# Kernel optimization log

Measured on AMD Instinct MI355X. Metric: run time of the kernel, lower is better.

Reference implementation:

```python
import jax, jax.numpy as jnp
import numpy as np

MUL = 32          # multiplicity of 0e and 1o in edge_messages_irreps
E = 40000         # number of edges
NODE_DIM = 128    # 128x0e node feats
EDGE_DIM = 32     # 32x0e edge feats
WEIGHT_NUMEL = 5 * MUL * MUL  # 5 uvu instructions, (u,v)=(32,32) weights each

# Levi-Civita tensor = sqrt(6) * wigner_3j(1,1,1) in the e3nn real basis
_eps = np.zeros((3, 3, 3), np.float32)
for a, b, c in [(0, 1, 2), (1, 2, 0), (2, 0, 1)]:
    _eps[a, b, c] = 1.0
    _eps[a, c, b] = -1.0
EPS = jnp.asarray(_eps)


def setup_inputs() -> dict:
    key = jax.random.key(0)
    ks = jax.random.split(key, 13)
    return {
        "edge_feats": jax.random.normal(ks[0], (E, EDGE_DIM), jnp.float32),
        "edge_messages1": jax.random.normal(ks[1], (E, 4 * MUL), jnp.float32),
        "edge_messages2": jax.random.normal(ks[2], (E, 4 * MUL), jnp.float32),
        "node_feats_sender": jax.random.normal(ks[3], (E, NODE_DIM), jnp.float32),
        "node_feats_receiver": jax.random.normal(ks[4], (E, NODE_DIM), jnp.float32),
        "W_nodes": jax.random.normal(ks[5], (NODE_DIM, EDGE_DIM), jnp.float32),
        "W_mlp1": jax.random.normal(ks[6], (3 * EDGE_DIM, 128), jnp.float32),
        "W_mlp2": jax.random.normal(ks[7], (128, 128), jnp.float32),
        "W_mlp3": jax.random.normal(ks[8], (128, WEIGHT_NUMEL), jnp.float32),
        "W_out_0e": jax.random.normal(ks[9], (2 * MUL, MUL), jnp.float32),
        "W_out_1o": jax.random.normal(ks[10], (2 * MUL, MUL), jnp.float32),
        "W_out_1e": jax.random.normal(ks[11], (MUL, MUL), jnp.float32),
        "edge_index": jax.random.randint(ks[12], (2, E), 0, 10000, jnp.int64 if jax.config.jax_enable_x64 else jnp.int32),
    }


def reference(edge_feats, edge_messages1, edge_messages2, node_feats_sender,
              node_feats_receiver, W_nodes, W_mlp1, W_mlp2, W_mlp3,
              W_out_0e, W_out_1o, W_out_1e, edge_index):
    # nodes_linear: o3.Linear on pure scalars == dense matmul with 1/sqrt(fan_in)
    s_send = (node_feats_sender @ W_nodes) * (1.0 / np.sqrt(NODE_DIM))
    s_recv = (node_feats_receiver @ W_nodes) * (1.0 / np.sqrt(NODE_DIM))
    scal = jnp.concatenate([s_send, s_recv, edge_feats], axis=1)  # [E, 96]

    # FullyConnectedNet [96,128,128,weight_numel] with SiLU, e3nn fan-in scaling
    h = jax.nn.silu((scal @ W_mlp1) * (1.0 / np.sqrt(3 * EDGE_DIM)))
    h = jax.nn.silu((h @ W_mlp2) * (1.0 / np.sqrt(128)))
    w = (h @ W_mlp3) * (1.0 / np.sqrt(128))          # [E, 5120] per-edge TP weights
    w = w.reshape(-1, 5, MUL, MUL)                    # 5 uvu instructions

    # split messages into 32x0e scalars and 32x1o vectors
    x1_0 = edge_messages1[:, :MUL]
    x1_1 = edge_messages1[:, MUL:].reshape(-1, MUL, 3)
    x2_0 = edge_messages2[:, :MUL]
    x2_1 = edge_messages2[:, MUL:].reshape(-1, MUL, 3)

    # per-edge-weighted uvu tensor product; alpha = sqrt(ir_out.dim / fan) with
    # CG constants (1, d/sqrt(3), eps/sqrt(6)) folded in
    c1 = jnp.einsum('euv,eu,ev->eu', w[:, 0], x1_0, x2_0) * (1.0 / np.sqrt(MUL))          # 0e
    c2 = jnp.einsum('euv,eu,evj->euj', w[:, 1], x1_0, x2_1) * (1.0 / np.sqrt(MUL))        # 1o
    c3 = jnp.einsum('euv,eui,ev->eui', w[:, 2], x1_1, x2_0) * (1.0 / np.sqrt(MUL))        # 1o
    c4 = jnp.einsum('euv,eui,evi->eu', w[:, 3], x1_1, x2_1) * (1.0 / np.sqrt(3 * MUL))    # 0e
    c5 = jnp.einsum('euv,eui,evj,ijk->euk', w[:, 4], x1_1, x2_1, EPS) * (1.0 / np.sqrt(2 * MUL))  # 1e

    # output_linear: o3.Linear over irreps_mid -> 32x0e + 32x1o + 32x1e
    mid_0e = jnp.concatenate([c1, c4], axis=1)        # [E, 64]
    mid_1o = jnp.concatenate([c2, c3], axis=1)        # [E, 64, 3]
    out_0e = (mid_0e @ W_out_0e) * (1.0 / np.sqrt(2 * MUL))                      # [E, 32]
    out_1o = jnp.einsum('euj,uw->ewj', mid_1o, W_out_1o) * (1.0 / np.sqrt(2 * MUL))
    out_1e = jnp.einsum('euk,uw->ewk', c5, W_out_1e) * (1.0 / np.sqrt(MUL))

    n = out_0e.shape[0]
    return jnp.concatenate(
        [out_0e, out_1o.reshape(n, 3 * MUL), out_1e.reshape(n, 3 * MUL)], axis=1)  # [E, 224]
```

## Files before the change

### kernel.cpp

```cpp
#include <hip/hip_runtime.h>
#include <hip/hip_bf16.h>
#include <math.h>

typedef __attribute__((ext_vector_type(8)))  short bf16x8;
typedef __attribute__((ext_vector_type(4)))  float f32x4;
typedef __attribute__((ext_vector_type(16))) float f32x16;

#define S128 0.08838834764831845f
#define S96  0.10206207261596575f
#define S32  0.17677669529663687f
#define S64  0.125f
#define NE   40000

__device__ __forceinline__ float silu_f(float x){ return x / (1.0f + expf(-x)); }
__device__ __forceinline__ ushort f2b(float x){
    __hip_bfloat16 b = __float2bfloat16(x); return *(ushort*)&b;
}
__device__ __forceinline__ float b2f(ushort u){
    return __uint_as_float(((uint)u) << 16);
}
__device__ __forceinline__ float blo(uint d){ return __uint_as_float(d << 16); }
__device__ __forceinline__ float bhi(uint d){ return __uint_as_float(d & 0xffff0000u); }
__device__ __forceinline__ uint packbf(float a, float b){
    return (uint)f2b(a) | ((uint)f2b(b) << 16);
}

__global__ __launch_bounds__(256)
void prep_weights(const float* __restrict__ Wn, const float* __restrict__ W1,
                  const float* __restrict__ W2, ushort* __restrict__ WnT,
                  ushort* __restrict__ W1T, ushort* __restrict__ W2T) {
    int idx = blockIdx.x * 256 + threadIdx.x;
    if (idx < 4096) {
        int n = idx >> 7, k = idx & 127;
        WnT[n * 128 + k] = f2b(Wn[k * 32 + n]);
    } else if (idx < 16384) {
        int t = idx - 4096; int n = t / 96, k = t - n * 96;
        W1T[n * 96 + k] = f2b(W1[k * 128 + n]);
    } else {
        int t = idx - 16384; int n = t >> 7, k = t & 127;
        W2T[n * 128 + k] = f2b(W2[k * 128 + n]);
    }
}

__global__ __launch_bounds__(256)
void w3_fragpack(const float* __restrict__ W3, ushort* __restrict__ w3A) {
    const int pu = blockIdx.x;
    const int t  = threadIdx.x;
    #pragma unroll
    for (int s = 0; s < 2; ++s) {
        int slot = s * 256 + t;
        int ks = slot >> 6, l = slot & 63;
        int m = pu * 32 + (l & 31);
        int kbase = ks * 16 + (l >> 5) * 8;
        bf16x8 v;
        #pragma unroll
        for (int i = 0; i < 8; ++i)
            v[i] = (short)f2b(W3[(size_t)(kbase + i) * 5120 + m]);
        *(bf16x8*)&w3A[((size_t)(pu * 8 + ks) * 64 + l) * 8] = v;
    }
}

__global__ __launch_bounds__(512, 6)
void mega2(const float* __restrict__ ef,  const float* __restrict__ em2,
           const float* __restrict__ nfs, const float* __restrict__ nfr,
           const ushort* __restrict__ WnT, const ushort* __restrict__ W1T,
           const ushort* __restrict__ W2T, const ushort* __restrict__ w3A,
           ushort* __restrict__ dt)
{
    __shared__ __align__(16) ushort scratch[15360];
    __shared__ __align__(16) ushort hbuf[64 * 128];

    const int tid  = threadIdx.x;
    const int lane = tid & 63, wv = tid >> 6;
    const int l15  = lane & 15, lg = lane >> 4;
    const int e0   = blockIdx.x * 64;

    ushort* scal = scratch;
    ushort* h1b  = scratch + 6656;
    uint*   xp2  = (uint*)scratch;

    #pragma unroll
    for (int q = 0; q < 4; ++q) {
        int idx = q * 512 + tid;
        int e = idx >> 5, j = idx & 31;
        scal[e * 104 + 64 + j] = f2b(ef[(size_t)(e0 + e) * 32 + j]);
    }

    {
        const int h = wv >> 2, eb = (wv & 3) * 16;
        const float* src = h ? nfr : nfs;
        const size_t erow = (size_t)(e0 + eb + l15) * 128;
        f32x4 acc1[2] = {{0,0,0,0},{0,0,0,0}};
        #pragma unroll
        for (int ks = 0; ks < 4; ++ks) {
            float4 va = *(const float4*)(src + erow + ks * 32 + lg * 8);
            float4 vb = *(const float4*)(src + erow + ks * 32 + lg * 8 + 4);
            bf16x8 a;
            a[0]=(short)f2b(va.x); a[1]=(short)f2b(va.y);
            a[2]=(short)f2b(va.z); a[3]=(short)f2b(va.w);
            a[4]=(short)f2b(vb.x); a[5]=(short)f2b(vb.y);
            a[6]=(short)f2b(vb.z); a[7]=(short)f2b(vb.w);
            #pragma unroll
            for (int nf = 0; nf < 2; ++nf) {
                bf16x8 b = *(const bf16x8*)(WnT + (nf * 16 + l15) * 128 + ks * 32 + lg * 8);
                acc1[nf] = __builtin_amdgcn_mfma_f32_16x16x32_bf16(a, b, acc1[nf], 0, 0, 0);
            }
        }
        #pragma unroll
        for (int nf = 0; nf < 2; ++nf)
            #pragma unroll
            for (int r = 0; r < 4; ++r)
                scal[(eb + lg * 4 + r) * 104 + h * 32 + nf * 16 + l15] =
                    f2b(acc1[nf][r] * S128);
    }
    __syncthreads();

    {
        const int et = wv & 3, nh = wv >> 2;
        f32x4 acc2[4] = {{0,0,0,0},{0,0,0,0},{0,0,0,0},{0,0,0,0}};
        #pragma unroll
        for (int ks = 0; ks < 3; ++ks) {
            bf16x8 a = *(const bf16x8*)&scal[(et * 16 + l15) * 104 + ks * 32 + lg * 8];
            #pragma unroll
            for (int nf = 0; nf < 4; ++nf) {
                int gn = nh * 4 + nf;
                bf16x8 b = *(const bf16x8*)(W1T + (gn * 16 + l15) * 96 + ks * 32 + lg * 8);
                acc2[nf] = __builtin_amdgcn_mfma_f32_16x16x32_bf16(a, b, acc2[nf], 0, 0, 0);
            }
        }
        #pragma unroll
        for (int nf = 0; nf < 4; ++nf)
            #pragma unroll
            for (int r = 0; r < 4; ++r)
                h1b[(et * 16 + lg * 4 + r) * 136 + (nh * 4 + nf) * 16 + l15] =
                    f2b(silu_f(acc2[nf][r] * S96));
    }
    __syncthreads();

    {
        const int et = wv & 3, nh = wv >> 2;
        f32x4 acc3[4] = {{0,0,0,0},{0,0,0,0},{0,0,0,0},{0,0,0,0}};
        #pragma unroll
        for (int ks = 0; ks < 4; ++ks) {
            bf16x8 a = *(const bf16x8*)&h1b[(et * 16 + l15) * 136 + ks * 32 + lg * 8];
            #pragma unroll
            for (int nf = 0; nf < 4; ++nf) {
                int gn = nh * 4 + nf;
                bf16x8 b = *(const bf16x8*)(W2T + (gn * 16 + l15) * 128 + ks * 32 + lg * 8);
                acc3[nf] = __builtin_amdgcn_mfma_f32_16x16x32_bf16(a, b, acc3[nf], 0, 0, 0);
            }
        }
        __syncthreads();
        #pragma unroll
        for (int nf = 0; nf < 4; ++nf)
            #pragma unroll
            for (int r = 0; r < 4; ++r) {
                int e = et * 16 + lg * 4 + r;
                int col = (nh * 4 + nf) * 16 + l15;
                hbuf[e * 128 + (col ^ ((e & 15) << 3))] =
                    f2b(silu_f(acc3[nf][r] * S128));
            }
    }

    {
        int part = tid >> 7;
        int sub  = tid & 127;
        int e = sub >> 1, hi2 = sub & 1;
        const float* xr = em2 + (size_t)(e0 + e) * 128;
        uint* dst = &xp2[(hi2 * 64 + e) * 34];
        if (part == 0) {
            #pragma unroll
            for (int g = 0; g < 4; ++g)
                #pragma unroll
                for (int c = 0; c < 2; ++c) {
                    int v0 = 8 * g + 4 * hi2 + 2 * c;
                    float2 t1 = *(const float2*)(xr + v0);
                    dst[g * 2 + c] = packbf(t1.x, t1.y);
                }
        } else {
            int j = part - 1;
            #pragma unroll
            for (int g = 0; g < 4; ++g)
                #pragma unroll
                for (int c = 0; c < 2; ++c) {
                    int v0 = 8 * g + 4 * hi2 + 2 * c;
                    dst[8 + j * 8 + g * 2 + c] =
                        packbf(xr[32 + v0 * 3 + j], xr[32 + (v0 + 1) * 3 + j]);
                }
        }
    }
    __syncthreads();

    const int el  = lane & 31;
    const int hi  = lane >> 5;
    const int sw0 = (el & 15) << 3;

    #pragma unroll 1
    for (int un = 0; un < 20; ++un) {
        const int pu = un * 8 + wv;
        const int p = pu >> 5, u = pu & 31;
        const ushort* Ab = w3A + (size_t)pu * 4096 + lane * 8;

        bf16x8 a[8];
        #pragma unroll
        for (int ks = 0; ks < 8; ++ks)
            a[ks] = *(const bf16x8*)(Ab + ks * 512);

        #pragma unroll 1
        for (int eh = 0; eh < 2; ++eh) {
            const int ebase = e0 + eh * 32;
            const ushort* hrow = &hbuf[(eh * 32 + el) * 128];
            f32x16 acc = {0,0,0,0,0,0,0,0,0,0,0,0,0,0,0,0};
            #pragma unroll
            for (int ks = 0; ks < 8; ++ks) {
                bf16x8 b = *(const bf16x8*)&hrow[(ks * 16 + hi * 8) ^ sw0];
                acc = __builtin_amdgcn_mfma_f32_32x32x16_bf16(a[ks], b, acc, 0, 0, 0);
            }
            const uint* xb = &xp2[(hi * 64 + eh * 32 + el) * 34];
            if (p == 0 || p == 2) {
                const int row = ((p == 0) ? 0 : 128) + u;
                float s = 0.f;
                #pragma unroll
                for (int g = 0; g < 4; ++g) {
                    uint2 q = *(const uint2*)&xb[g * 2];
                    s += acc[g*4+0]*blo(q.x) + acc[g*4+1]*bhi(q.x)
                       + acc[g*4+2]*blo(q.y) + acc[g*4+3]*bhi(q.y);
                }
                s += __shfl_xor(s, 32);
                if (hi == 0)
                    dt[(size_t)row * NE + ebase + el] = f2b(s * S128);
            } else {
                const int row0 = ((p == 1) ? 32 : (p == 3) ? 160 : 256) + u * 3;
                float sj[3];
                #pragma unroll
                for (int j = 0; j < 3; ++j) {
                    float s = 0.f;
                    #pragma unroll
                    for (int g = 0; g < 4; ++g) {
                        uint2 q = *(const uint2*)&xb[8 + j * 8 + g * 2];
                        s += acc[g*4+0]*blo(q.x) + acc[g*4+1]*bhi(q.x)
                           + acc[g*4+2]*blo(q.y) + acc[g*4+3]*bhi(q.y);
                    }
                    s += __shfl_xor(s, 32);
                    sj[j] = s;
                }
                if (hi == 0) {
                    #pragma unroll
                    for (int j = 0; j < 3; ++j)
                        dt[(size_t)(row0 + j) * NE + ebase + el] = f2b(sj[j] * S128);
                }
            }
        }
    }
}

__global__ __launch_bounds__(256)
void finalize2(const float* __restrict__ em1, const ushort* __restrict__ dt,
               const float* __restrict__ W0e, const float* __restrict__ W1o,
               const float* __restrict__ W1e, float* __restrict__ out)
{
    __shared__ __align__(16) ushort dl[352 * 33];
    __shared__ __align__(16) ushort x1b[32 * 132];
    const int tid  = threadIdx.x;
    const int lane = tid & 63, wv = tid >> 6;
    const int l15  = lane & 15, lg = lane >> 4;
    const int eb   = blockIdx.x * 32;

    for (int idx = tid; idx < 352 * 32; idx += 256) {
        int row = idx >> 5, e = idx & 31;
        dl[row * 33 + e] = dt[(size_t)row * NE + eb + e];
    }
    {
        int e = tid >> 3, seg = tid & 7;
        const float* x1 = em1 + (size_t)(eb + e) * 128 + seg * 16;
        #pragma unroll
        for (int q = 0; q < 4; ++q) {
            float4 v = *(const float4*)(x1 + q * 4);
            *(uint*)&x1b[e * 132 + seg * 16 + q * 4]     = packbf(v.x, v.y);
            *(uint*)&x1b[e * 132 + seg * 16 + q * 4 + 2] = packbf(v.z, v.w);
        }
    }
    __syncthreads();

    #pragma unroll 1
    for (int it = 0; it < 4; ++it) {
        int unit = it * 4 + wv;
        if (unit >= 14) break;
        int mi = unit & 1, task = unit >> 1;
        const int ei = mi * 16 + l15;
        const ushort* xe = &x1b[ei * 132];
        const size_t orow = (size_t)(eb + mi * 16 + lg * 4) * 224;

        if (task == 0) {
            bf16x8 af0, af1;
            #pragma unroll
            for (int t = 0; t < 8; ++t) {
                int u = lg * 8 + t;
                af0[t] = (short)f2b(S32 * b2f(xe[u]) * b2f(dl[u * 33 + ei]));
                float c4 = 0.f;
                #pragma unroll
                for (int i = 0; i < 3; ++i)
                    c4 += b2f(xe[32 + u * 3 + i]) * b2f(dl[(160 + u * 3 + i) * 33 + ei]);
                af1[t] = (short)f2b(c4 * S96);
            }
            #pragma unroll
            for (int nf = 0; nf < 2; ++nf) {
                bf16x8 bf0, bf1;
                #pragma unroll
                for (int t = 0; t < 8; ++t) {
                    bf0[t] = (short)f2b(W0e[(lg * 8 + t) * 32 + nf * 16 + l15]);
                    bf1[t] = (short)f2b(W0e[(32 + lg * 8 + t) * 32 + nf * 16 + l15]);
                }
                f32x4 o = {0.f, 0.f, 0.f, 0.f};
                o = __builtin_amdgcn_mfma_f32_16x16x32_bf16(af0, bf0, o, 0, 0, 0);
                o = __builtin_amdgcn_mfma_f32_16x16x32_bf16(af1, bf1, o, 0, 0, 0);
                #pragma unroll
                for (int rr = 0; rr < 4; ++rr)
                    out[orow + (size_t)rr * 224 + nf * 16 + l15] = o[rr] * S64;
            }
        } else if (task <= 3) {
            int j = task - 1;
            bf16x8 af0, af1;
            #pragma unroll
            for (int t = 0; t < 8; ++t) {
                int u = lg * 8 + t;
                af0[t] = (short)f2b(S32 * b2f(xe[u]) * b2f(dl[(32 + u * 3 + j) * 33 + ei]));
                af1[t] = (short)f2b(S32 * b2f(xe[32 + u * 3 + j]) * b2f(dl[(128 + u) * 33 + ei]));
            }
            #pragma unroll
            for (int nf = 0; nf < 2; ++nf) {
                bf16x8 bf0, bf1;
                #pragma unroll
                for (int t = 0; t < 8; ++t) {
                    bf0[t] = (short)f2b(W1o[(lg * 8 + t) * 32 + nf * 16 + l15]);
                    bf1[t] = (short)f2b(W1o[(32 + lg * 8 + t) * 32 + nf * 16 + l15]);
                }
                f32x4 o = {0.f, 0.f, 0.f, 0.f};
                o = __builtin_amdgcn_mfma_f32_16x16x32_bf16(af0, bf0, o, 0, 0, 0);
                o = __builtin_amdgcn_mfma_f32_16x16x32_bf16(af1, bf1, o, 0, 0, 0);
                #pragma unroll
                for (int rr = 0; rr < 4; ++rr)
                    out[orow + (size_t)rr * 224 + 32 + (nf * 16 + l15) * 3 + j] = o[rr] * S64;
            }
        } else {
            int k = task - 4;
            int k1 = k + 1; if (k1 > 2) k1 -= 3;
            int k2 = k + 2; if (k2 > 2) k2 -= 3;
            bf16x8 af0;
            #pragma unroll
            for (int t = 0; t < 8; ++t) {
                int u = lg * 8 + t;
                float a_ = b2f(xe[32 + u * 3 + k1]) * b2f(dl[(256 + u * 3 + k2) * 33 + ei])
                         - b2f(xe[32 + u * 3 + k2]) * b2f(dl[(256 + u * 3 + k1) * 33 + ei]);
                af0[t] = (short)f2b(a_ * S64);
            }
            #pragma unroll
            for (int nf = 0; nf < 2; ++nf) {
                bf16x8 bf0;
                #pragma unroll
                for (int t = 0; t < 8; ++t)
                    bf0[t] = (short)f2b(W1e[(lg * 8 + t) * 32 + nf * 16 + l15]);
                f32x4 o = {0.f, 0.f, 0.f, 0.f};
                o = __builtin_amdgcn_mfma_f32_16x16x32_bf16(af0, bf0, o, 0, 0, 0);
                #pragma unroll
                for (int rr = 0; rr < 4; ++rr)
                    out[orow + (size_t)rr * 224 + 128 + (nf * 16 + l15) * 3 + k] = o[rr] * S32;
            }
        }
    }
}

extern "C" void kernel_launch(void* const* d_in, const int* in_sizes, int n_in,
                              void* d_out, int out_size, void* d_ws, size_t ws_size,
                              hipStream_t stream) {
    const float* ef  = (const float*)d_in[0];
    const float* em1 = (const float*)d_in[1];
    const float* em2 = (const float*)d_in[2];
    const float* nfs = (const float*)d_in[3];
    const float* nfr = (const float*)d_in[4];
    const float* Wn  = (const float*)d_in[5];
    const float* W1  = (const float*)d_in[6];
    const float* W2  = (const float*)d_in[7];
    const float* W3  = (const float*)d_in[8];
    const float* W0e = (const float*)d_in[9];
    const float* W1o = (const float*)d_in[10];
    const float* W1e = (const float*)d_in[11];
    float* out = (float*)d_out;

    const int E = in_sizes[0] / 32;

    char* ws = (char*)d_ws;
    ushort* w3A = (ushort*)ws;
    size_t off = (size_t)5120 * 128 * 2;
    ushort* WnT = (ushort*)(ws + off);  off += 32 * 128 * 2;
    ushort* W1T = (ushort*)(ws + off);  off += 128 * 96 * 2;
    ushort* W2T = (ushort*)(ws + off);  off += 128 * 128 * 2;
    ushort* dt  = (ushort*)(ws + off);

    prep_weights<<<128, 256, 0, stream>>>(Wn, W1, W2, WnT, W1T, W2T);
    w3_fragpack<<<160, 256, 0, stream>>>(W3, w3A);
    mega2<<<E / 64, 512, 0, stream>>>(ef, em2, nfs, nfr,
                                      WnT, W1T, W2T, w3A, dt);
    finalize2<<<E / 32, 256, 0, stream>>>(em1, dt, W0e, W1o, W1e, out);
}
```

Measured before the change: 152.1 us.

## Double-buffer W3 fragments, keep hbuf B operands in registers, store x2 as fp32

The mega kernel's main loop now loads the W3 A-fragments for the next unit while the MFMAs for the current unit run, using two register buffers. The hidden-state B fragments are loaded once into registers instead of being reread from LDS on every unit. The em2 staging keeps fp32 values in a new layout instead of packed bf16, which removes the unpack arithmetic and raises precision. The extra registers force launch bounds down from 6 to 4 waves, and LDS use grows, so occupancy drops.

Measured after the change: 320.6 us. 2.11x slower.

```diff
diff --git a/kernel.cpp b/kernel.cpp
--- a/kernel.cpp
+++ b/kernel.cpp
@@ -19,8 +19,6 @@
 __device__ __forceinline__ float b2f(ushort u){
     return __uint_as_float(((uint)u) << 16);
 }
-__device__ __forceinline__ float blo(uint d){ return __uint_as_float(d << 16); }
-__device__ __forceinline__ float bhi(uint d){ return __uint_as_float(d & 0xffff0000u); }
 __device__ __forceinline__ uint packbf(float a, float b){
     return (uint)f2b(a) | ((uint)f2b(b) << 16);
 }
@@ -60,14 +58,14 @@
     }
 }
 
-__global__ __launch_bounds__(512, 6)
-void mega2(const float* __restrict__ ef,  const float* __restrict__ em2,
+__global__ __launch_bounds__(512, 4)
+void mega3(const float* __restrict__ ef,  const float* __restrict__ em2,
            const float* __restrict__ nfs, const float* __restrict__ nfr,
            const ushort* __restrict__ WnT, const ushort* __restrict__ W1T,
            const ushort* __restrict__ W2T, const ushort* __restrict__ w3A,
            ushort* __restrict__ dt)
 {
-    __shared__ __align__(16) ushort scratch[15360];
+    __shared__ __align__(16) ushort scratch[16640];
     __shared__ __align__(16) ushort hbuf[64 * 128];
 
     const int tid  = threadIdx.x;
@@ -77,7 +75,7 @@
 
     ushort* scal = scratch;
     ushort* h1b  = scratch + 6656;
-    uint*   xp2  = (uint*)scratch;
+    float*  x2f  = (float*)scratch;
 
     #pragma unroll
     for (int q = 0; q < 4; ++q) {
@@ -163,30 +161,24 @@
     }
 
     {
-        int part = tid >> 7;
-        int sub  = tid & 127;
-        int e = sub >> 1, hi2 = sub & 1;
+        int e = tid >> 3, grp = tid & 7;
         const float* xr = em2 + (size_t)(e0 + e) * 128;
-        uint* dst = &xp2[(hi2 * 64 + e) * 34];
-        if (part == 0) {
-            #pragma unroll
-            for (int g = 0; g < 4; ++g)
-                #pragma unroll
-                for (int c = 0; c < 2; ++c) {
-                    int v0 = 8 * g + 4 * hi2 + 2 * c;
-                    float2 t1 = *(const float2*)(xr + v0);
-                    dst[g * 2 + c] = packbf(t1.x, t1.y);
-                }
-        } else {
-            int j = part - 1;
-            #pragma unroll
-            for (int g = 0; g < 4; ++g)
-                #pragma unroll
-                for (int c = 0; c < 2; ++c) {
-                    int v0 = 8 * g + 4 * hi2 + 2 * c;
-                    dst[8 + j * 8 + g * 2 + c] =
-                        packbf(xr[32 + v0 * 3 + j], xr[32 + (v0 + 1) * 3 + j]);
-                }
+        float* dst = &x2f[e * 130];
+        #pragma unroll
+        for (int r = 0; r < 16; ++r) {
+            int idx = grp * 16 + r;
+            int reg = idx & 15;
+            int vb = (reg & 3) + 8 * (reg >> 2);
+            float val;
+            if (idx < 32) {
+                int hi2 = idx >> 4;
+                val = xr[vb + 4 * hi2];
+            } else {
+                int slot = (idx - 32) >> 4;
+                int j = slot >> 1, hi2 = slot & 1;
+                val = xr[32 + (vb + 4 * hi2) * 3 + j];
+            }
+            dst[idx] = val;
         }
     }
     __syncthreads();
@@ -195,62 +187,74 @@
     const int hi  = lane >> 5;
     const int sw0 = (el & 15) << 3;
 
-    #pragma unroll 1
-    for (int un = 0; un < 20; ++un) {
-        const int pu = un * 8 + wv;
+    bf16x8 B[2][8];
+    #pragma unroll
+    for (int eh = 0; eh < 2; ++eh)
+        #pragma unroll
+        for (int ks = 0; ks < 8; ++ks)
+            B[eh][ks] = *(const bf16x8*)&hbuf[(eh * 32 + el) * 128
+                                              + ((ks * 16 + hi * 8) ^ sw0)];
+    const float* x2r0 = &x2f[el * 130];
+    const float* x2r1 = &x2f[(32 + el) * 130];
+
+    auto compute = [&](const bf16x8 (&a)[8], int pu) {
         const int p = pu >> 5, u = pu & 31;
-        const ushort* Ab = w3A + (size_t)pu * 4096 + lane * 8;
-
-        bf16x8 a[8];
-        #pragma unroll
-        for (int ks = 0; ks < 8; ++ks)
-            a[ks] = *(const bf16x8*)(Ab + ks * 512);
-
-        #pragma unroll 1
+        #pragma unroll
         for (int eh = 0; eh < 2; ++eh) {
-            const int ebase = e0 + eh * 32;
-            const ushort* hrow = &hbuf[(eh * 32 + el) * 128];
             f32x16 acc = {0,0,0,0,0,0,0,0,0,0,0,0,0,0,0,0};
             #pragma unroll
-            for (int ks = 0; ks < 8; ++ks) {
-                bf16x8 b = *(const bf16x8*)&hrow[(ks * 16 + hi * 8) ^ sw0];
-                acc = __builtin_amdgcn_mfma_f32_32x32x16_bf16(a[ks], b, acc, 0, 0, 0);
-            }
-            const uint* xb = &xp2[(hi * 64 + eh * 32 + el) * 34];
+            for (int ks = 0; ks < 8; ++ks)
+                acc = __builtin_amdgcn_mfma_f32_32x32x16_bf16(a[ks], B[eh][ks], acc, 0, 0, 0);
+            const float* xr = eh ? x2r1 : x2r0;
+            const int ecol = e0 + eh * 32 + el;
             if (p == 0 || p == 2) {
-                const int row = ((p == 0) ? 0 : 128) + u;
                 float s = 0.f;
                 #pragma unroll
-                for (int g = 0; g < 4; ++g) {
-                    uint2 q = *(const uint2*)&xb[g * 2];
-                    s += acc[g*4+0]*blo(q.x) + acc[g*4+1]*bhi(q.x)
-                       + acc[g*4+2]*blo(q.y) + acc[g*4+3]*bhi(q.y);
+                for (int g = 0; g < 8; ++g) {
+                    float2 q = *(const float2*)&xr[hi * 16 + g * 2];
+                    s += acc[2*g] * q.x + acc[2*g+1] * q.y;
                 }
                 s += __shfl_xor(s, 32);
                 if (hi == 0)
-                    dt[(size_t)row * NE + ebase + el] = f2b(s * S128);
+                    dt[(size_t)(((p == 0) ? 0 : 128) + u) * NE + ecol] = f2b(s * S128);
             } else {
                 const int row0 = ((p == 1) ? 32 : (p == 3) ? 160 : 256) + u * 3;
-                float sj[3];
                 #pragma unroll
                 for (int j = 0; j < 3; ++j) {
                     float s = 0.f;
                     #pragma unroll
-                    for (int g = 0; g < 4; ++g) {
-                        uint2 q = *(const uint2*)&xb[8 + j * 8 + g * 2];
-                        s += acc[g*4+0]*blo(q.x) + acc[g*4+1]*bhi(q.x)
-                           + acc[g*4+2]*blo(q.y) + acc[g*4+3]*bhi(q.y);
+                    for (int g = 0; g < 8; ++g) {
+                        float2 q = *(const float2*)&xr[32 + (j * 2 + hi) * 16 + g * 2];
+                        s += acc[2*g] * q.x + acc[2*g+1] * q.y;
                     }
                     s += __shfl_xor(s, 32);
-                    sj[j] = s;
+                    if (hi == 0)
+                        dt[(size_t)(row0 + j) * NE + ecol] = f2b(s * S128);
                 }
-                if (hi == 0) {
-                    #pragma unroll
-                    for (int j = 0; j < 3; ++j)
-                        dt[(size_t)(row0 + j) * NE + ebase + el] = f2b(sj[j] * S128);
-                }
-            }
-        }
+            }
+        }
+    };
+
+    bf16x8 aA[8], aB[8];
+    {
+        const ushort* Ab = w3A + (size_t)(0 * 8 + wv) * 4096 + lane * 8;
+        #pragma unroll
+        for (int ks = 0; ks < 8; ++ks) aA[ks] = *(const bf16x8*)(Ab + ks * 512);
+    }
+    #pragma unroll 1
+    for (int ub = 0; ub < 20; ub += 2) {
+        {
+            const ushort* Ab = w3A + (size_t)((ub + 1) * 8 + wv) * 4096 + lane * 8;
+            #pragma unroll
+            for (int ks = 0; ks < 8; ++ks) aB[ks] = *(const bf16x8*)(Ab + ks * 512);
+        }
+        compute(aA, ub * 8 + wv);
+        if (ub + 2 < 20) {
+            const ushort* Ab = w3A + (size_t)((ub + 2) * 8 + wv) * 4096 + lane * 8;
+            #pragma unroll
+            for (int ks = 0; ks < 8; ++ks) aA[ks] = *(const bf16x8*)(Ab + ks * 512);
+        }
+        compute(aB, (ub + 1) * 8 + wv);
     }
 }
 
@@ -399,7 +403,7 @@
 
     prep_weights<<<128, 256, 0, stream>>>(Wn, W1, W2, WnT, W1T, W2T);
     w3_fragpack<<<160, 256, 0, stream>>>(W3, w3A);
-    mega2<<<E / 64, 512, 0, stream>>>(ef, em2, nfs, nfr,
+    mega3<<<E / 64, 512, 0, stream>>>(ef, em2, nfs, nfr,
                                       WnT, W1T, W2T, w3A, dt);
     finalize2<<<E / 32, 256, 0, stream>>>(em1, dt, W0e, W1o, W1e, out);
 }
```
